# Optimization experiments

Measured on AMD Instinct MI355X. Metric: run time of the kernel, lower is better.

## Reference

```python
import jax, jax.numpy as jnp
import numpy as np

S = 16          # state_dim
H = 96          # hidden_dim
A = 64          # num_actions
B = 256         # batch_size
D_IN = S * S * 64      # 16384
D_H = H * H            # 9216
SPLIT = D_H - S * S    # 8960, action/selection split point


def setup_inputs() -> dict:
    key = jax.random.key(0)
    ks = jax.random.split(key, 14)
    s = jax.random.normal(ks[0], (B, S, S, 64), dtype=jnp.float32)
    mask = jax.random.randint(ks[1], (B, S, S), 0, 2).astype(bool)
    u = jax.random.uniform(ks[2], (B, S * S), dtype=jnp.float32,
                           minval=1e-6, maxval=1.0 - 1e-6)
    def lin(k, fin, fout):
        kw, kb = jax.random.split(k)
        sc = 1.0 / np.sqrt(fin)
        return (jax.random.uniform(kw, (fin, fout), minval=-sc, maxval=sc, dtype=jnp.float32),
                jax.random.uniform(kb, (fout,), minval=-sc, maxval=sc, dtype=jnp.float32))
    W1, b1 = lin(ks[3], D_IN, D_H)
    W2, b2 = lin(ks[4], D_H, D_H)
    W3, b3 = lin(ks[5], D_H, D_H)
    Wa, ba = lin(ks[6], SPLIT, A)
    Ws, bs = lin(ks[7], S * S, S * S)
    return {"s": s, "mask": mask, "u": u, "W1": W1, "b1": b1, "W2": W2,
            "b2": b2, "W3": W3, "b3": b3, "Wa": Wa, "ba": ba, "Ws": Ws, "bs": bs}


def reference(s, mask, u, W1, b1, W2, b2, W3, b3, Wa, ba, Ws, bs):
    x = s.reshape(s.shape[0], -1).astype(jnp.float32)        # [B, D_IN]
    x = jax.nn.relu(x @ W1 + b1)                             # [B, D_H]
    x = jax.nn.relu(x @ W2 + b2)
    x = jax.nn.relu(x @ W3 + b3)
    x_action = jax.nn.softmax(x[:, :SPLIT] @ Wa + ba, axis=1)  # [B, A]
    # selection branch
    p = jax.nn.softmax(x[:, SPLIT:] @ Ws + bs, axis=1)         # [B, S*S]
    m = mask.reshape(mask.shape[0], -1)                        # [B, S*S]
    p = jnp.where(m, -1e9, p)        # masked_fill on the probs (faithful)
    p = jax.nn.softmax(p, axis=1)
    # parallel Gumbel-max == Categorical over valid (unnormalized) probs
    gumbel = -jnp.log(-jnp.log(u))
    scores = jnp.where(m, -jnp.inf, jnp.log(p) + gumbel)
    idx = jnp.argmax(scores, axis=1)                           # [B]
    coordinate = jnp.stack([idx // S, idx % S], axis=1)        # [B, 2]
    sel_prob = jnp.take_along_axis(p, idx[:, None], axis=1)    # [B, 1]
    final_action_prob = x_action * sel_prob                    # [B, A]
    return final_action_prob, coordinate
```

## Files before the change

kernel.cpp:

```cpp
#include <hip/hip_runtime.h>
#include <hip/hip_fp16.h>


typedef _Float16 f16;
typedef _Float16 f16x4 __attribute__((ext_vector_type(4)));
typedef _Float16 f16x8 __attribute__((ext_vector_type(8)));
typedef float f32x4 __attribute__((ext_vector_type(4)));

#define DH 9216
#define SPLIT 8960

__device__ __forceinline__ void gload16(const void* g, void* l) {
    __builtin_amdgcn_global_load_lds(
        (const __attribute__((address_space(1))) void*)g,
        (__attribute__((address_space(3))) void*)l, 16, 0, 0);
}

__global__ void cvt_kernel(const float* __restrict__ in, f16* __restrict__ out, int n) {
    for (int i = (blockIdx.x * blockDim.x + threadIdx.x) * 4; i < n;
         i += gridDim.x * blockDim.x * 4) {
        float4 v = *(const float4*)(in + i);
        f16x4 h = {(_Float16)v.x, (_Float16)v.y, (_Float16)v.z, (_Float16)v.w};
        *(f16x4*)(out + i) = h;
    }
}

__global__ __launch_bounds__(256, 3) void gemm_kernel(
    const f16* __restrict__ A, int K, int Kh, int yshift,
    const float* __restrict__ W,
    float* __restrict__ P)
{
    __shared__ __align__(16) char stageMem[2][24576];
    const int bid  = blockIdx.x;
    const int y    = bid & ((1 << yshift) - 1);
    const int n0   = (bid >> yshift) * 64;
    const int tid  = threadIdx.x;
    const int lane = tid & 63;
    const int wid  = tid >> 6;
    const int kbase = y * Kh;
    const int ns   = Kh >> 5;

    f32x4 acc[4][4] = {};

    auto stage_issue = [&](int st, int t) {
        char* sw = &stageMem[st][0];
        const int kt = kbase + (t << 5);
#pragma unroll
        for (int r = 0; r < 2; ++r) {
            int g = tid + (r << 8);
            int k = g >> 4, cg = g & 15;
            const float* src = W + (size_t)(kt + k) * DH + n0 + ((cg ^ ((k >> 3) << 2)) << 2);
            gload16(src, sw + g * 16);
        }
#pragma unroll
        for (int r = 0; r < 4; ++r) {
            int g = tid + (r << 8);
            int row = g >> 2, kg = g & 3;
            const f16* srcA = A + (size_t)row * K + kt + (kg << 3);
            gload16(srcA, sw + 8192 + g * 16);
        }
    };

    stage_issue(0, 0);
    stage_issue(1, 1);
    __builtin_amdgcn_sched_barrier(0);

    for (int t = 0; t < ns; ++t) {
        const int st = t & 1;
        if (t + 1 < ns) asm volatile("s_waitcnt vmcnt(6)" ::: "memory");
        else            asm volatile("s_waitcnt vmcnt(0)" ::: "memory");
        __builtin_amdgcn_s_barrier();
        __builtin_amdgcn_sched_barrier(0);

        const float* wlds = (const float*)&stageMem[st][0];
        const f16*   alds = (const f16*)&stageMem[st][8192];

        f16x8 af[4], bf[4];
#pragma unroll
        for (int ri = 0; ri < 4; ++ri) {
            int row = wid * 64 + ri * 16 + (lane & 15);
            af[ri] = *(const f16x8*)(alds + row * 32 + ((lane >> 4) << 3));
        }
        const int xork  = (lane >> 4) << 2;
        const int basek = (lane >> 4) << 3;
#pragma unroll
        for (int ni = 0; ni < 4; ++ni) {
            int cg = (ni << 2) + ((lane & 15) >> 2);
            int dw = (basek << 6) + ((cg ^ xork) << 2) + (lane & 3);
            float wv[8];
#pragma unroll
            for (int j = 0; j < 8; ++j) wv[j] = wlds[dw + (j << 6)];
            f16x8 b;
#pragma unroll
            for (int j = 0; j < 8; ++j) b[j] = (_Float16)wv[j];
            bf[ni] = b;
        }
#pragma unroll
        for (int ri = 0; ri < 4; ++ri)
#pragma unroll
            for (int ni = 0; ni < 4; ++ni)
                acc[ri][ni] = __builtin_amdgcn_mfma_f32_16x16x32_f16(
                    af[ri], bf[ni], acc[ri][ni], 0, 0, 0);

        asm volatile("s_waitcnt lgkmcnt(0)" ::: "memory");
        __builtin_amdgcn_sched_barrier(0);
        __builtin_amdgcn_s_barrier();
        __builtin_amdgcn_sched_barrier(0);
        if (t + 2 < ns) {
            stage_issue(st, t + 2);
            __builtin_amdgcn_sched_barrier(0);
        }
    }

    float* Pb = P + (size_t)y * (256 * DH);
#pragma unroll
    for (int ri = 0; ri < 4; ++ri) {
        int row = wid * 64 + ri * 16 + ((lane >> 4) << 2);
#pragma unroll
        for (int ni = 0; ni < 4; ++ni) {
            int col = n0 + ni * 16 + (lane & 15);
#pragma unroll
            for (int rg = 0; rg < 4; ++rg)
                Pb[(size_t)(row + rg) * DH + col] = acc[ri][ni][rg];
        }
    }
}

__global__ void reduce_kernel(const float* __restrict__ P, int S,
                              const float* __restrict__ bias,
                              f16* __restrict__ oh, float* __restrict__ out32) {
    const int n = 256 * DH;
    for (int i = (blockIdx.x * blockDim.x + threadIdx.x) * 4; i < n;
         i += gridDim.x * blockDim.x * 4) {
        float4 bb = *(const float4*)(bias + (i % DH));
        float4 r = bb;
        for (int j = 0; j < S; ++j) {
            float4 a = *(const float4*)(P + (size_t)j * n + i);
            r.x += a.x; r.y += a.y; r.z += a.z; r.w += a.w;
        }
        r.x = fmaxf(r.x, 0.f); r.y = fmaxf(r.y, 0.f);
        r.z = fmaxf(r.z, 0.f); r.w = fmaxf(r.w, 0.f);
        if (oh) {
            f16x4 h = {(_Float16)r.x, (_Float16)r.y, (_Float16)r.z, (_Float16)r.w};
            *(f16x4*)(oh + i) = h;
        }
        if (out32) *(float4*)(out32 + i) = r;
    }
}

__global__ __launch_bounds__(256) void action_kernel(
    const float* __restrict__ X3, const float* __restrict__ Wa,
    const float* __restrict__ ba, float* __restrict__ xact) {
    __shared__ float xs[SPLIT];
    __shared__ float red[256];
    const int row = blockIdx.x, t = threadIdx.x;
    const float* xr = X3 + (size_t)row * DH;
    for (int k = t * 4; k < SPLIT; k += 1024)
        *(float4*)&xs[k] = *(const float4*)(xr + k);
    __syncthreads();
    const int col = t & 63, kqq = t >> 6;
    float acc = 0.f;
    for (int k = kqq * 2240; k < (kqq + 1) * 2240; ++k)
        acc += xs[k] * Wa[(size_t)k * 64 + col];
    red[t] = acc;
    __syncthreads();
    if (t < 64) {
        float z = red[t] + red[t + 64] + red[t + 128] + red[t + 192] + ba[t];
        float mx = z;
        for (int off = 32; off; off >>= 1) mx = fmaxf(mx, __shfl_xor(mx, off));
        float e = expf(z - mx);
        float s = e;
        for (int off = 32; off; off >>= 1) s += __shfl_xor(s, off);
        xact[row * 64 + t] = e / s;
    }
}

__global__ __launch_bounds__(256) void select_kernel(
    const float* __restrict__ X3, const float* __restrict__ Ws,
    const float* __restrict__ bs, const void* __restrict__ maskp,
    const float* __restrict__ u, const float* __restrict__ xact,
    float* __restrict__ out) {
    __shared__ float xs[256];
    __shared__ float psh[256];
    __shared__ float rr[4];
    __shared__ float bestv[4];
    __shared__ int besti[4];
    __shared__ int sIdx;
    __shared__ int smode;
    const int row = blockIdx.x, t = threadIdx.x;
    const int lane = t & 63, wid = t >> 6;

    if (t < 64) {
        unsigned v = ((const unsigned*)maskp)[t];
        int okInt  = __all(v <= 1u);
        int okByte = __all((v & 0xFEFEFEFEu) == 0u);
        if (t == 0) smode = okInt ? 0 : (okByte ? 1 : 2);
    }
    xs[t] = X3[(size_t)row * DH + SPLIT + t];
    __syncthreads();

    bool mk;
    if (smode == 0)       mk = ((const int*)maskp)[row * 256 + t] != 0;
    else if (smode == 1)  mk = ((const unsigned char*)maskp)[row * 256 + t] != 0;
    else                  mk = ((const float*)maskp)[row * 256 + t] != 0.0f;

    float z = bs[t];
    for (int k = 0; k < 256; ++k)
        z += xs[k] * Ws[k * 256 + t];

    float v = z;
    for (int off = 32; off; off >>= 1) v = fmaxf(v, __shfl_xor(v, off));
    if (lane == 0) rr[wid] = v;
    __syncthreads();
    float m1 = fmaxf(fmaxf(rr[0], rr[1]), fmaxf(rr[2], rr[3]));
    __syncthreads();
    float e1 = expf(z - m1);
    v = e1;
    for (int off = 32; off; off >>= 1) v += __shfl_xor(v, off);
    if (lane == 0) rr[wid] = v;
    __syncthreads();
    float s1 = rr[0] + rr[1] + rr[2] + rr[3];
    __syncthreads();
    float p1 = e1 / s1;

    float q = mk ? -1e9f : p1;
    v = q;
    for (int off = 32; off; off >>= 1) v = fmaxf(v, __shfl_xor(v, off));
    if (lane == 0) rr[wid] = v;
    __syncthreads();
    float m2 = fmaxf(fmaxf(rr[0], rr[1]), fmaxf(rr[2], rr[3]));
    __syncthreads();
    float e2 = expf(q - m2);
    v = e2;
    for (int off = 32; off; off >>= 1) v += __shfl_xor(v, off);
    if (lane == 0) rr[wid] = v;
    __syncthreads();
    float s2 = rr[0] + rr[1] + rr[2] + rr[3];
    float p2 = e2 / s2;
    psh[t] = p2;

    float g = -logf(-logf(u[row * 256 + t]));
    float sc = mk ? -INFINITY : (logf(p2) + g);
    float bv = sc;
    int bi = t;
    for (int off = 32; off; off >>= 1) {
        float ov = __shfl_xor(bv, off);
        int oi = __shfl_xor(bi, off);
        if (ov > bv || (ov == bv && oi < bi)) { bv = ov; bi = oi; }
    }
    if (lane == 0) { bestv[wid] = bv; besti[wid] = bi; }
    __syncthreads();
    if (t == 0) {
        float fv = bestv[0];
        int fi = besti[0];
        for (int w = 1; w < 4; ++w)
            if (bestv[w] > fv || (bestv[w] == fv && besti[w] < fi)) {
                fv = bestv[w]; fi = besti[w];
            }
        sIdx = fi;
    }
    __syncthreads();
    const int idx = sIdx;
    const float sp = psh[idx];
    if (t < 64) out[row * 64 + t] = xact[row * 64 + t] * sp;
    if (t == 0) {
        out[256 * 64 + row * 2 + 0] = (float)(idx >> 4);
        out[256 * 64 + row * 2 + 1] = (float)(idx & 15);
    }
}

extern "C" void kernel_launch(void* const* d_in, const int* in_sizes, int n_in,
                              void* d_out, int out_size, void* d_ws, size_t ws_size,
                              hipStream_t stream) {
    const float* s  = (const float*)d_in[0];
    const void*  mask = d_in[1];
    const float* u  = (const float*)d_in[2];
    const float* W1 = (const float*)d_in[3];
    const float* b1 = (const float*)d_in[4];
    const float* W2 = (const float*)d_in[5];
    const float* b2 = (const float*)d_in[6];
    const float* W3 = (const float*)d_in[7];
    const float* b3 = (const float*)d_in[8];
    const float* Wa = (const float*)d_in[9];
    const float* ba = (const float*)d_in[10];
    const float* Ws = (const float*)d_in[11];
    const float* bs = (const float*)d_in[12];
    float* out = (float*)d_out;
    char* ws = (char*)d_ws;

    f16*   A0 = (f16*)(ws + 0);
    f16*   X1 = (f16*)(ws + 8388608);
    f16*   X2 = (f16*)(ws + 0);
    float* X3 = (float*)(ws + 13107200);
    float* XA = (float*)(ws + 22544384);
    float* P  = (float*)(ws + 22609920);

    const size_t pbytes = 9437184ull;
    int yshift = (ws_size >= 22609920ull + 8 * pbytes) ? 3 : 2;
    const int S = 1 << yshift;

    cvt_kernel<<<2048, 256, 0, stream>>>(s, A0, 256 * 16384);

    const int nblk = 144 * S;
    gemm_kernel<<<nblk, 256, 0, stream>>>(A0, 16384, 16384 / S, yshift, W1, P);
    reduce_kernel<<<1152, 256, 0, stream>>>(P, S, b1, X1, nullptr);
    gemm_kernel<<<nblk, 256, 0, stream>>>(X1, DH, DH / S, yshift, W2, P);
    reduce_kernel<<<1152, 256, 0, stream>>>(P, S, b2, X2, nullptr);
    gemm_kernel<<<nblk, 256, 0, stream>>>(X2, DH, DH / S, yshift, W3, P);
    reduce_kernel<<<1152, 256, 0, stream>>>(P, S, b3, nullptr, X3);

    action_kernel<<<256, 256, 0, stream>>>(X3, Wa, ba, XA);
    select_kernel<<<256, 256, 0, stream>>>(X3, Ws, bs, mask, u, XA, out);
}
```

Baseline: 605.8 us.

## Load activations directly to registers and shrink GEMM block to two waves

The split-K GEMM now uses 128-thread blocks, with each wave covering 128 rows (8x4 MFMA tiles) instead of 64. Activation fragments are loaded straight from global memory into registers, double-buffered in even/odd sets, rather than staged through LDS. Only the fp32 weight tile goes through LDS, now with a new XOR swizzle. This cuts LDS traffic and footprint and removes the activation LDS round trip, at the cost of much higher register pressure (128 accumulator floats plus 16 A vectors) and fewer waves per block to hide latency.

```diff
diff --git a/kernel.cpp b/kernel.cpp
--- a/kernel.cpp
+++ b/kernel.cpp
@@ -25,12 +25,12 @@
     }
 }
 
-__global__ __launch_bounds__(256, 3) void gemm_kernel(
+__global__ __launch_bounds__(128, 2) void gemm_kernel(
     const f16* __restrict__ A, int K, int Kh, int yshift,
     const float* __restrict__ W,
     float* __restrict__ P)
 {
-    __shared__ __align__(16) char stageMem[2][24576];
+    __shared__ __align__(16) char wlds[2][8192];
     const int bid  = blockIdx.x;
     const int y    = bid & ((1 << yshift) - 1);
     const int n0   = (bid >> yshift) * 64;
@@ -40,82 +40,88 @@
     const int kbase = y * Kh;
     const int ns   = Kh >> 5;
 
-    f32x4 acc[4][4] = {};
-
-    auto stage_issue = [&](int st, int t) {
-        char* sw = &stageMem[st][0];
+    f32x4 acc[8][4] = {};
+    f16x8 aE[8], aO[8];
+
+    auto issueW = [&](int slot, int t) {
+        char* dst = &wlds[slot][0];
         const int kt = kbase + (t << 5);
 #pragma unroll
-        for (int r = 0; r < 2; ++r) {
-            int g = tid + (r << 8);
-            int k = g >> 4, cg = g & 15;
-            const float* src = W + (size_t)(kt + k) * DH + n0 + ((cg ^ ((k >> 3) << 2)) << 2);
-            gload16(src, sw + g * 16);
-        }
-#pragma unroll
         for (int r = 0; r < 4; ++r) {
-            int g = tid + (r << 8);
-            int row = g >> 2, kg = g & 3;
-            const f16* srcA = A + (size_t)row * K + kt + (kg << 3);
-            gload16(srcA, sw + 8192 + g * 16);
+            int g = tid + (r << 7);
+            int k = g >> 4, x = g & 15;
+            int cg = x ^ (((k >> 3) * 5) & 15);
+            const float* src = W + (size_t)(kt + k) * DH + n0 + (cg << 2);
+            gload16(src, dst + g * 16);
         }
     };
-
-    stage_issue(0, 0);
-    stage_issue(1, 1);
-    __builtin_amdgcn_sched_barrier(0);
-
-    for (int t = 0; t < ns; ++t) {
-        const int st = t & 1;
-        if (t + 1 < ns) asm volatile("s_waitcnt vmcnt(6)" ::: "memory");
-        else            asm volatile("s_waitcnt vmcnt(0)" ::: "memory");
-        __builtin_amdgcn_s_barrier();
-        __builtin_amdgcn_sched_barrier(0);
-
-        const float* wlds = (const float*)&stageMem[st][0];
-        const f16*   alds = (const f16*)&stageMem[st][8192];
-
-        f16x8 af[4], bf[4];
-#pragma unroll
-        for (int ri = 0; ri < 4; ++ri) {
-            int row = wid * 64 + ri * 16 + (lane & 15);
-            af[ri] = *(const f16x8*)(alds + row * 32 + ((lane >> 4) << 3));
-        }
-        const int xork  = (lane >> 4) << 2;
-        const int basek = (lane >> 4) << 3;
+    auto loadA = [&](f16x8* a, int t) {
+        const int k0 = kbase + (t << 5) + ((lane >> 4) << 3);
+        const f16* base = A + (size_t)(wid * 128 + (lane & 15)) * K + k0;
+#pragma unroll
+        for (int ri = 0; ri < 8; ++ri)
+            a[ri] = *(const f16x8*)(base + (size_t)(ri * 16) * K);
+    };
+    auto mfma_step = [&](int slot, f16x8* a) {
+        const float* wl = (const float*)&wlds[slot][0];
+        const int r = lane >> 4;
+        f16x8 bf[4];
 #pragma unroll
         for (int ni = 0; ni < 4; ++ni) {
-            int cg = (ni << 2) + ((lane & 15) >> 2);
-            int dw = (basek << 6) + ((cg ^ xork) << 2) + (lane & 3);
-            float wv[8];
-#pragma unroll
-            for (int j = 0; j < 8; ++j) wv[j] = wlds[dw + (j << 6)];
+            int c = ni * 16 + (lane & 15);
+            int pos = ((((c >> 2) ^ (r * 5)) & 15) << 2) + (c & 3);
             f16x8 b;
 #pragma unroll
-            for (int j = 0; j < 8; ++j) b[j] = (_Float16)wv[j];
+            for (int j = 0; j < 8; ++j)
+                b[j] = (_Float16)wl[(r * 8 + j) * 64 + pos];
             bf[ni] = b;
         }
 #pragma unroll
-        for (int ri = 0; ri < 4; ++ri)
+        for (int ri = 0; ri < 8; ++ri)
 #pragma unroll
             for (int ni = 0; ni < 4; ++ni)
                 acc[ri][ni] = __builtin_amdgcn_mfma_f32_16x16x32_f16(
-                    af[ri], bf[ni], acc[ri][ni], 0, 0, 0);
-
+                    a[ri], bf[ni], acc[ri][ni], 0, 0, 0);
+    };
+
+    issueW(0, 0); loadA(aE, 0);
+    issueW(1, 1); loadA(aO, 1);
+    __builtin_amdgcn_sched_barrier(0);
+
+    for (int t = 0; t < ns; t += 2) {
+        asm volatile("s_waitcnt vmcnt(12)" ::: "memory");
+        __builtin_amdgcn_sched_barrier(0);
+        __builtin_amdgcn_s_barrier();
+        __builtin_amdgcn_sched_barrier(0);
+        mfma_step(0, aE);
+        if (t + 2 < ns) loadA(aE, t + 2);
+        __builtin_amdgcn_sched_barrier(0);
         asm volatile("s_waitcnt lgkmcnt(0)" ::: "memory");
         __builtin_amdgcn_sched_barrier(0);
         __builtin_amdgcn_s_barrier();
         __builtin_amdgcn_sched_barrier(0);
-        if (t + 2 < ns) {
-            stage_issue(st, t + 2);
-            __builtin_amdgcn_sched_barrier(0);
-        }
+        if (t + 2 < ns) issueW(0, t + 2);
+        __builtin_amdgcn_sched_barrier(0);
+        if (t + 2 < ns) asm volatile("s_waitcnt vmcnt(12)" ::: "memory");
+        else            asm volatile("s_waitcnt vmcnt(0)"  ::: "memory");
+        __builtin_amdgcn_sched_barrier(0);
+        __builtin_amdgcn_s_barrier();
+        __builtin_amdgcn_sched_barrier(0);
+        mfma_step(1, aO);
+        if (t + 3 < ns) loadA(aO, t + 3);
+        __builtin_amdgcn_sched_barrier(0);
+        asm volatile("s_waitcnt lgkmcnt(0)" ::: "memory");
+        __builtin_amdgcn_sched_barrier(0);
+        __builtin_amdgcn_s_barrier();
+        __builtin_amdgcn_sched_barrier(0);
+        if (t + 3 < ns) issueW(1, t + 3);
+        __builtin_amdgcn_sched_barrier(0);
     }
 
     float* Pb = P + (size_t)y * (256 * DH);
 #pragma unroll
-    for (int ri = 0; ri < 4; ++ri) {
-        int row = wid * 64 + ri * 16 + ((lane >> 4) << 2);
+    for (int ri = 0; ri < 8; ++ri) {
+        int row = wid * 128 + ri * 16 + ((lane >> 4) << 2);
 #pragma unroll
         for (int ni = 0; ni < 4; ++ni) {
             int col = n0 + ni * 16 + (lane & 15);
@@ -302,11 +308,11 @@
     cvt_kernel<<<2048, 256, 0, stream>>>(s, A0, 256 * 16384);
 
     const int nblk = 144 * S;
-    gemm_kernel<<<nblk, 256, 0, stream>>>(A0, 16384, 16384 / S, yshift, W1, P);
+    gemm_kernel<<<nblk, 128, 0, stream>>>(A0, 16384, 16384 / S, yshift, W1, P);
     reduce_kernel<<<1152, 256, 0, stream>>>(P, S, b1, X1, nullptr);
-    gemm_kernel<<<nblk, 256, 0, stream>>>(X1, DH, DH / S, yshift, W2, P);
+    gemm_kernel<<<nblk, 128, 0, stream>>>(X1, DH, DH / S, yshift, W2, P);
     reduce_kernel<<<1152, 256, 0, stream>>>(P, S, b2, X2, nullptr);
-    gemm_kernel<<<nblk, 256, 0, stream>>>(X2, DH, DH / S, yshift, W3, P);
+    gemm_kernel<<<nblk, 128, 0, stream>>>(X2, DH, DH / S, yshift, W3, P);
     reduce_kernel<<<1152, 256, 0, stream>>>(P, S, b3, nullptr, X3);
 
     action_kernel<<<256, 256, 0, stream>>>(X3, Wa, ba, XA);
```

Measured after the change: 694.5 us. +14.6%, slower.

## Widen GEMM block tile to 256x128 with 2x2 warp layout

Applied to the files above, without the earlier changes.

The split-K GEMM block tile grows from 64 to 128 output columns. The four waves are arranged 2x2, each computing 128 rows by 64 columns, so every A tile loaded into LDS is reused across twice as many columns, and the LDS swizzle is changed to an XOR pattern based on 5*k. The grid is halved, LDS per block grows to 64KB, and launch bounds drop to 2 blocks per CU. This trades occupancy and more accumulator registers for less redundant A traffic and more MFMA work per barrier.

```diff
diff --git a/kernel.cpp b/kernel.cpp
--- a/kernel.cpp
+++ b/kernel.cpp
@@ -25,100 +25,99 @@
     }
 }
 
-__global__ __launch_bounds__(256, 3) void gemm_kernel(
+__global__ __launch_bounds__(256, 2) void gemm_kernel(
     const f16* __restrict__ A, int K, int Kh, int yshift,
     const float* __restrict__ W,
     float* __restrict__ P)
 {
-    __shared__ __align__(16) char stageMem[2][24576];
+    __shared__ __align__(16) char lds[2][32768];
     const int bid  = blockIdx.x;
     const int y    = bid & ((1 << yshift) - 1);
-    const int n0   = (bid >> yshift) * 64;
+    const int n0   = (bid >> yshift) * 128;
     const int tid  = threadIdx.x;
     const int lane = tid & 63;
     const int wid  = tid >> 6;
+    const int wm   = wid >> 1, wn = wid & 1;
     const int kbase = y * Kh;
     const int ns   = Kh >> 5;
 
-    f32x4 acc[4][4] = {};
-
-    auto stage_issue = [&](int st, int t) {
-        char* sw = &stageMem[st][0];
+    f32x4 acc[8][4] = {};
+
+    auto issue = [&](int slot, int t) {
+        char* dst = &lds[slot][0];
         const int kt = kbase + (t << 5);
 #pragma unroll
-        for (int r = 0; r < 2; ++r) {
-            int g = tid + (r << 8);
-            int k = g >> 4, cg = g & 15;
-            const float* src = W + (size_t)(kt + k) * DH + n0 + ((cg ^ ((k >> 3) << 2)) << 2);
-            gload16(src, sw + g * 16);
-        }
-#pragma unroll
         for (int r = 0; r < 4; ++r) {
-            int g = tid + (r << 8);
-            int row = g >> 2, kg = g & 3;
-            const f16* srcA = A + (size_t)row * K + kt + (kg << 3);
-            gload16(srcA, sw + 8192 + g * 16);
-        }
+            int g = (r << 8) + tid;
+            int k = g >> 5, p = g & 31;
+            int cg = p ^ ((5 * (k >> 3)) & 31);
+            gload16(W + (size_t)(kt + k) * DH + n0 + (cg << 2), dst + g * 16);
+        }
+#pragma unroll
+        for (int r = 0; r < 4; ++r)
+            gload16(A + (size_t)tid * K + kt + (r << 3),
+                    dst + 16384 + (r << 12) + tid * 16);
     };
 
-    stage_issue(0, 0);
-    stage_issue(1, 1);
-    __builtin_amdgcn_sched_barrier(0);
-
-    for (int t = 0; t < ns; ++t) {
-        const int st = t & 1;
-        if (t + 1 < ns) asm volatile("s_waitcnt vmcnt(6)" ::: "memory");
-        else            asm volatile("s_waitcnt vmcnt(0)" ::: "memory");
-        __builtin_amdgcn_s_barrier();
-        __builtin_amdgcn_sched_barrier(0);
-
-        const float* wlds = (const float*)&stageMem[st][0];
-        const f16*   alds = (const f16*)&stageMem[st][8192];
-
-        f16x8 af[4], bf[4];
-#pragma unroll
-        for (int ri = 0; ri < 4; ++ri) {
-            int row = wid * 64 + ri * 16 + (lane & 15);
-            af[ri] = *(const f16x8*)(alds + row * 32 + ((lane >> 4) << 3));
-        }
-        const int xork  = (lane >> 4) << 2;
-        const int basek = (lane >> 4) << 3;
+    auto step = [&](int slot) {
+        const float* wl = (const float*)&lds[slot][0];
+        const f16*   al = (const f16*)&lds[slot][16384];
+        const int q  = lane >> 4;
+        const int lc = lane & 15;
+        f16x8 af[8], bf[4];
+#pragma unroll
+        for (int ri = 0; ri < 8; ++ri) {
+            int row = wm * 128 + ri * 16 + lc;
+            af[ri] = *(const f16x8*)(al + (q << 11) + (row << 3));
+        }
+        const int xw = (5 * q) & 31;
 #pragma unroll
         for (int ni = 0; ni < 4; ++ni) {
-            int cg = (ni << 2) + ((lane & 15) >> 2);
-            int dw = (basek << 6) + ((cg ^ xork) << 2) + (lane & 3);
-            float wv[8];
-#pragma unroll
-            for (int j = 0; j < 8; ++j) wv[j] = wlds[dw + (j << 6)];
+            int c  = wn * 64 + ni * 16 + lc;
+            int fi = (((c >> 2) ^ xw) << 2) + (c & 3);
             f16x8 b;
 #pragma unroll
-            for (int j = 0; j < 8; ++j) b[j] = (_Float16)wv[j];
+            for (int j = 0; j < 8; ++j)
+                b[j] = (_Float16)wl[(((q << 3) + j) << 7) + fi];
             bf[ni] = b;
         }
 #pragma unroll
-        for (int ri = 0; ri < 4; ++ri)
+        for (int ri = 0; ri < 8; ++ri)
 #pragma unroll
             for (int ni = 0; ni < 4; ++ni)
                 acc[ri][ni] = __builtin_amdgcn_mfma_f32_16x16x32_f16(
                     af[ri], bf[ni], acc[ri][ni], 0, 0, 0);
-
+    };
+
+    issue(0, 0);
+    issue(1, 1);
+    __builtin_amdgcn_sched_barrier(0);
+
+    for (int t = 0; t < ns; ++t) {
+        if (t + 1 < ns) asm volatile("s_waitcnt vmcnt(8)" ::: "memory");
+        else            asm volatile("s_waitcnt vmcnt(0)" ::: "memory");
+        __builtin_amdgcn_sched_barrier(0);
+        __builtin_amdgcn_s_barrier();
+        __builtin_amdgcn_sched_barrier(0);
+        step(t & 1);
+        __builtin_amdgcn_sched_barrier(0);
         asm volatile("s_waitcnt lgkmcnt(0)" ::: "memory");
         __builtin_amdgcn_sched_barrier(0);
         __builtin_amdgcn_s_barrier();
         __builtin_amdgcn_sched_barrier(0);
         if (t + 2 < ns) {
-            stage_issue(st, t + 2);
+            issue(t & 1, t + 2);
             __builtin_amdgcn_sched_barrier(0);
         }
     }
 
     float* Pb = P + (size_t)y * (256 * DH);
 #pragma unroll
-    for (int ri = 0; ri < 4; ++ri) {
-        int row = wid * 64 + ri * 16 + ((lane >> 4) << 2);
+    for (int ri = 0; ri < 8; ++ri) {
+        int row = wm * 128 + ri * 16 + ((lane >> 4) << 2);
 #pragma unroll
         for (int ni = 0; ni < 4; ++ni) {
-            int col = n0 + ni * 16 + (lane & 15);
+            int col = n0 + wn * 64 + ni * 16 + (lane & 15);
 #pragma unroll
             for (int rg = 0; rg < 4; ++rg)
                 Pb[(size_t)(row + rg) * DH + col] = acc[ri][ni][rg];
@@ -301,7 +300,7 @@
 
     cvt_kernel<<<2048, 256, 0, stream>>>(s, A0, 256 * 16384);
 
-    const int nblk = 144 * S;
+    const int nblk = 72 << yshift;
     gemm_kernel<<<nblk, 256, 0, stream>>>(A0, 16384, 16384 / S, yshift, W1, P);
     reduce_kernel<<<1152, 256, 0, stream>>>(P, S, b1, X1, nullptr);
     gemm_kernel<<<nblk, 256, 0, stream>>>(X1, DH, DH / S, yshift, W2, P);
```

New measurement: 655.7 us. +8.2%, slower.
